# Performance work log

Hardware: AMD Instinct MI355X
Metric: run time of the kernel (lower is better)

## Reference

```python
import jax, jax.numpy as jnp
import numpy as np

B = 4096
T_STEPS = 2048


def setup_inputs() -> dict:
    key = jax.random.key(0)
    k1, k2, k3 = jax.random.split(key, 3)
    inputs = jax.random.normal(k1, (B, T_STEPS), dtype=jnp.float32)
    # replicate torch init: params = rand(t); params /= sum(|params|); alternate signs
    p = jax.random.uniform(k2, (T_STEPS,), dtype=jnp.float32)
    p = p / jnp.sum(jnp.abs(p))
    sign = jnp.where(jnp.arange(T_STEPS) % 2 == 0, jnp.float32(1.0), jnp.float32(-1.0))
    params = p * sign
    bias = jax.random.normal(k3, (1,), dtype=jnp.float32)
    return {"inputs": inputs, "params": params, "bias": bias}


def reference(inputs, params, bias):
    """AR(t) recurrence: for i in [t, 2t): x_i = sum_j x_{i-1-j} * params[j] + bias.
    inputs: [B, t] seed values; returns the t generated values per row, [B, t].
    """
    t_steps = params.shape[0]
    # torch.dot uses inputs reversed (newest first) against params, so the
    # window kept in oldest->newest order pairs with reversed params.
    p_rev = params[::-1]

    def step(window, _):
        # window: [B, t] last t values, oldest -> newest
        new = window @ p_rev + bias[0]  # [B]
        window = jnp.concatenate([window[:, 1:], new[:, None]], axis=1)
        return window, new

    _, outs = jax.lax.scan(step, inputs, None, length=t_steps)
    return outs.T  # [B, t_steps]
```

## Files before the change

kernel.cpp:

```cpp
#include <hip/hip_runtime.h>
#include <hip/hip_bf16.h>

typedef _Float16 f16;
typedef _Float16 f16x8 __attribute__((ext_vector_type(8)));
typedef float f32x4 __attribute__((ext_vector_type(4)));

constexpr int TS = 2048;
constexpr int BB = 4096;

__device__ __forceinline__ int swz4(int c) { return c ^ ((c >> 3) & 7); }

struct ToepShared { char Xs[16384]; char Ws[8192]; };

template <bool REV>
__device__ void toep_body(ToepShared& lds, int w, const f16* __restrict__ Xg,
                          const char* __restrict__ Wg,
                          const float* __restrict__ biasp, void* __restrict__ Yg) {
  char* Xs = lds.Xs;
  char* Ws = lds.Ws;
  const int tid = threadIdx.x;
  const int lane = tid & 63;
  const int wid = tid >> 6;
  const int wrow = (wid >> 1) * 64;
  const int wcol = (wid & 1) * 32;
  const int px = w & 15;
  const int b0 = (w >> 4) * 128;

  float binit = 0.0f;
  if (REV) binit = biasp[0];

  for (int phase = 0; phase < 2; ++phase) {
    const int mblk = phase ? (31 - px) : px;
    const int m0 = mblk * 64;
    const int k0b = REV ? m0 : 0;
    const int k0e = REV ? TS : (m0 + 64);

    f32x4 acc[4][2];
    #pragma unroll
    for (int i = 0; i < 4; ++i)
      #pragma unroll
      for (int j = 0; j < 2; ++j) acc[i][j] = {binit, binit, binit, binit};

    for (int k0 = k0b; k0 < k0e; k0 += 64) {
      __syncthreads();
      #pragma unroll
      for (int t2 = 0; t2 < 4; ++t2) {
        const int t = wid * 4 + t2;
        const int row = t * 8 + (lane >> 3);
        const char* src = (const char*)Xg + ((size_t)(b0 + row) * TS + k0) * 2
                          + (((lane & 7) * 16) ^ ((row & 7) << 4));
        __builtin_amdgcn_global_load_lds(
            (const __attribute__((address_space(1))) unsigned int*)src,
            (__attribute__((address_space(3))) unsigned int*)(Xs + t * 1024),
            16, 0, 0);
      }
      const int dlt = (REV ? (k0 - m0) : (m0 - k0)) >> 6;
      const char* wsrc = Wg + (size_t)dlt * 8192;
      #pragma unroll
      for (int p = 0; p < 2; ++p) {
        const int t = wid * 2 + p;
        __builtin_amdgcn_global_load_lds(
            (const __attribute__((address_space(1))) unsigned int*)(wsrc + t * 1024 + lane * 16),
            (__attribute__((address_space(3))) unsigned int*)(Ws + t * 1024),
            16, 0, 0);
      }
      __syncthreads();

      #pragma unroll
      for (int ks = 0; ks < 2; ++ks) {
        const int colb = ks * 64 + ((lane >> 4) * 16);
        f16x8 af[4], bf[2];
        #pragma unroll
        for (int i = 0; i < 4; ++i) {
          const int row = wrow + i * 16 + (lane & 15);
          af[i] = *(const f16x8*)(Xs + row * 128 + (colb ^ ((row & 7) << 4)));
        }
        #pragma unroll
        for (int j = 0; j < 2; ++j) {
          const int n = wcol + j * 16 + (lane & 15);
          bf[j] = *(const f16x8*)(Ws + n * 128 + (colb ^ ((n & 7) << 4)));
        }
        #pragma unroll
        for (int i = 0; i < 4; ++i)
          #pragma unroll
          for (int j = 0; j < 2; ++j)
            acc[i][j] = __builtin_amdgcn_mfma_f32_16x16x32_f16(
                af[i], bf[j], acc[i][j], 0, 0, 0);
      }
    }

    #pragma unroll
    for (int i = 0; i < 4; ++i) {
      #pragma unroll
      for (int j = 0; j < 2; ++j) {
        #pragma unroll
        for (int r = 0; r < 4; ++r) {
          const int row = b0 + wrow + i * 16 + (lane >> 4) * 4 + r;
          const int col = m0 + wcol + j * 16 + (lane & 15);
          if (REV)
            ((f16*)Yg)[(size_t)row * TS + col] = (f16)acc[i][j][r];
          else
            ((float*)Yg)[(size_t)row * TS + col] = acc[i][j][r];
        }
      }
    }
  }
}

__global__ __launch_bounds__(1024) void prep_kernel(
    const float* __restrict__ X, f16* __restrict__ Xh,
    const float* __restrict__ params, char* __restrict__ Wg) {
  const int b = blockIdx.x;
  const int tid = threadIdx.x;

  if (b < 512) {
    const size_t base = ((size_t)b * 1024 + tid) * 16;
    const float4 a0 = *(const float4*)&X[base];
    const float4 a1 = *(const float4*)&X[base + 4];
    const float4 a2 = *(const float4*)&X[base + 8];
    const float4 a3 = *(const float4*)&X[base + 12];
    f16x8 v0 = {(f16)a0.x, (f16)a0.y, (f16)a0.z, (f16)a0.w,
                (f16)a1.x, (f16)a1.y, (f16)a1.z, (f16)a1.w};
    f16x8 v1 = {(f16)a2.x, (f16)a2.y, (f16)a2.z, (f16)a2.w,
                (f16)a3.x, (f16)a3.y, (f16)a3.z, (f16)a3.w};
    *(f16x8*)&Xh[base] = v0;
    *(f16x8*)&Xh[base + 8] = v1;
    return;
  }

  if (b == 512) {
    const int s2 = tid & 255;
    const int n = s2 >> 2, kq = s2 & 3;
    for (int dlt = tid >> 8; dlt < 32; dlt += 4) {
      char* tile = Wg + (size_t)dlt * 8192;
      #pragma unroll
      for (int part = 0; part < 2; ++part) {
        const int k8 = kq * 16 + part * 8;
        f16x8 v;
        #pragma unroll
        for (int ii = 0; ii < 8; ++ii) {
          const int k = k8 + ii;
          const int dd = dlt * 64 + k - n;
          v[ii] = ((unsigned)dd < (unsigned)TS) ? (f16)params[2047 - dd] : (f16)0.0f;
        }
        *(f16x8*)(tile + n * 128 + ((2 * k8) ^ ((n & 7) << 4))) = v;
      }
    }
    return;
  }

  __shared__ __align__(16) float rp1[2048];
  __shared__ __align__(16) float h_s[2048];
  __shared__ __align__(16) float hist[1024];
  __shared__ __align__(16) float hb[2052];

  const int lane = tid & 63;
  const int wave = tid >> 6;

  if (tid < 512) {
    const int y = tid * 4;
    f32x4 v;
    v[0] = params[2046 - y];
    v[1] = params[2045 - y];
    v[2] = params[2044 - y];
    v[3] = (y + 3 < 2047) ? params[2043 - y] : 0.0f;
    *(f32x4*)&rp1[swz4(tid) * 4] = v;
  }
  __syncthreads();

  if (wave == 0) {
    float hv = (lane == 0) ? 1.0f : 0.0f;
    for (int m = 1; m < 32; ++m) {
      float partial = 0.0f;
      if (lane < m) {
        const int yi = 2047 - m + lane;
        partial = hv * rp1[swz4(yi >> 2) * 4 + (yi & 3)];
      }
      #pragma unroll
      for (int off = 32; off; off >>= 1) partial += __shfl_xor(partial, off);
      if (lane == m) hv = partial;
    }
    if (lane < 32) h_s[lane] = hv;
  }
  __syncthreads();

  const int sub = tid & 7;
  const int gi = tid >> 3;

  for (int n = 32; n < 2048; n <<= 1) {
    const int ng16 = n >> 4;
    const int T = (n >= 128) ? (n >> 7) : 1;

    if (gi < ng16) {
      float acc[16];
      #pragma unroll
      for (int j = 0; j < 16; ++j) acc[j] = 0.0f;
      const int ybase = (2047 - n) - gi * 16 - 15;
      for (int t = 0; t < T; ++t) {
        const int m16 = (sub + 8 * t) * 16;
        if (m16 < n) {
          const int c0 = (ybase + m16) >> 2;
          f32x4 wv[8];
          #pragma unroll
          for (int q = 0; q < 8; ++q) wv[q] = *(const f32x4*)&rp1[swz4(c0 + q) * 4];
          f32x4 hv4[4];
          #pragma unroll
          for (int q = 0; q < 4; ++q) hv4[q] = *(const f32x4*)&h_s[m16 + 4 * q];
          #pragma unroll
          for (int d = 0; d < 16; ++d) {
            const float hd = hv4[d >> 2][d & 3];
            #pragma unroll
            for (int j = 0; j < 16; ++j) {
              const int k = d - j + 15;
              acc[j] += hd * wv[k >> 2][k & 3];
            }
          }
        }
      }
      #pragma unroll
      for (int j = 0; j < 16; ++j) {
        acc[j] += __shfl_xor(acc[j], 1);
        acc[j] += __shfl_xor(acc[j], 2);
        acc[j] += __shfl_xor(acc[j], 4);
      }
      if (sub == 0) {
        #pragma unroll
        for (int q = 0; q < 4; ++q) {
          f32x4 v = {acc[4 * q], acc[4 * q + 1], acc[4 * q + 2], acc[4 * q + 3]};
          *(f32x4*)&hist[gi * 16 + 4 * q] = v;
        }
      }
    }
    __syncthreads();

    const int P = n + 3;
    const int nchunk = (2 * n + 4) >> 2;
    for (int c = tid; c < nchunk; c += 1024) {
      f32x4 v;
      #pragma unroll
      for (int q = 0; q < 4; ++q) {
        const int idx = 4 * c + q - P;
        v[q] = ((unsigned)idx < (unsigned)n) ? hist[idx] : 0.0f;
      }
      *(f32x4*)&hb[swz4(c) * 4] = v;
    }
    __syncthreads();

    if (gi < ng16) {
      float acc[16];
      #pragma unroll
      for (int j = 0; j < 16; ++j) acc[j] = 0.0f;
      int t_end = (gi >= sub) ? (((gi - sub) >> 3) + 1) : 0;
      if (t_end > T) t_end = T;
      const int ybase = P + gi * 16 - 15;
      for (int t = 0; t < t_end; ++t) {
        const int r16 = (sub + 8 * t) * 16;
        const int c0 = (ybase - r16) >> 2;
        f32x4 wv[8];
        #pragma unroll
        for (int q = 0; q < 8; ++q) wv[q] = *(const f32x4*)&hb[swz4(c0 + q) * 4];
        f32x4 hv4[4];
        #pragma unroll
        for (int q = 0; q < 4; ++q) hv4[q] = *(const f32x4*)&h_s[r16 + 4 * q];
        #pragma unroll
        for (int d = 0; d < 16; ++d) {
          const float hd = hv4[d >> 2][d & 3];
          #pragma unroll
          for (int j = 0; j < 16; ++j) {
            const int k = j - d + 15;
            acc[j] += hd * wv[k >> 2][k & 3];
          }
        }
      }
      #pragma unroll
      for (int j = 0; j < 16; ++j) {
        acc[j] += __shfl_xor(acc[j], 1);
        acc[j] += __shfl_xor(acc[j], 2);
        acc[j] += __shfl_xor(acc[j], 4);
      }
      if (sub == 0) {
        #pragma unroll
        for (int q = 0; q < 4; ++q) {
          f32x4 v = {acc[4 * q], acc[4 * q + 1], acc[4 * q + 2], acc[4 * q + 3]};
          *(f32x4*)&h_s[n + gi * 16 + 4 * q] = v;
        }
      }
    }
    __syncthreads();
  }

  {
    const int s2 = tid & 255;
    const int n2 = s2 >> 2, kq = s2 & 3;
    char* WgC = Wg + 32 * 8192;
    for (int dlt = tid >> 8; dlt < 32; dlt += 4) {
      char* tile = WgC + (size_t)dlt * 8192;
      #pragma unroll
      for (int part = 0; part < 2; ++part) {
        const int k8 = kq * 16 + part * 8;
        f16x8 v;
        #pragma unroll
        for (int ii = 0; ii < 8; ++ii) {
          const int k = k8 + ii;
          const int dd = dlt * 64 + n2 - k;
          v[ii] = ((unsigned)dd < (unsigned)TS) ? (f16)h_s[dd] : (f16)0.0f;
        }
        *(f16x8*)(tile + n2 * 128 + ((2 * k8) ^ ((n2 & 7) << 4))) = v;
      }
    }
  }
}

__global__ __launch_bounds__(256, 2) void toep_A(
    const f16* __restrict__ Xh, const char* __restrict__ Wg,
    const float* __restrict__ biasp, f16* __restrict__ u) {
  __shared__ ToepShared lds;
  const int b = blockIdx.x;
  toep_body<true>(lds, (b & 7) * 64 + (b >> 3), Xh, Wg, biasp, (void*)u);
}

__global__ __launch_bounds__(256, 2) void toep_C(
    const f16* __restrict__ u, const char* __restrict__ WgC,
    float* __restrict__ out) {
  __shared__ ToepShared lds;
  const int b = blockIdx.x;
  toep_body<false>(lds, (b & 7) * 64 + (b >> 3), u, WgC, nullptr, (void*)out);
}

extern "C" void kernel_launch(void* const* d_in, const int* in_sizes, int n_in,
                              void* d_out, int out_size, void* d_ws, size_t ws_size,
                              hipStream_t stream) {
  const float* inputs = (const float*)d_in[0];
  const float* params = (const float*)d_in[1];
  const float* bias   = (const float*)d_in[2];
  float* out = (float*)d_out;

  char* ws = (char*)d_ws;
  f16*  Xh = (f16*)ws;
  f16*  u  = (f16*)(ws + (size_t)BB * TS * 2);
  char* Wg = ws + (size_t)BB * TS * 4;

  prep_kernel<<<514, 1024, 0, stream>>>(inputs, Xh, params, Wg);
  toep_A<<<512, 256, 0, stream>>>(Xh, Wg, bias, u);
  toep_C<<<512, 256, 0, stream>>>(u, Wg + 32 * 8192, out);
}
```

Measured before the change: 113.3 us.

## Overlap impulse-response computation with first Toeplitz GEMM in one launch

The serial impulse-response (h) computation moves out of the prep kernel, where a single 1024-thread block was the critical path, into an extra block of the first Toeplitz GEMM kernel. It now runs on 256 threads concurrently with the GEMM tiles. The prep kernel is reshaped into 256-thread blocks, with a separate block per weight tile. Shared memory becomes a union sized to the larger h buffers (about 28KB), which may lower occupancy of the GEMM blocks. The h block with 256 threads may also become a long tail.

After: 118.2 us. +4.2%, slower.

```diff
diff --git a/kernel.cpp b/kernel.cpp
--- a/kernel.cpp
+++ b/kernel.cpp
@@ -11,6 +11,16 @@
 __device__ __forceinline__ int swz4(int c) { return c ^ ((c >> 3) & 7); }
 
 struct ToepShared { char Xs[16384]; char Ws[8192]; };
+
+union MegaShared {
+  ToepShared t;
+  struct {
+    float rp1[2048];
+    float h[2048];
+    float hist[1024];
+    float hbuf[2052];
+  } hb;
+};
 
 template <bool REV>
 __device__ void toep_body(ToepShared& lds, int w, const f16* __restrict__ Xg,
@@ -107,14 +117,174 @@
   }
 }
 
-__global__ __launch_bounds__(1024) void prep_kernel(
+__device__ void h_block_body(MegaShared& lds, const float* __restrict__ params,
+                             char* __restrict__ WgC) {
+  float* rp1 = lds.hb.rp1;
+  float* h_s = lds.hb.h;
+  float* hist = lds.hb.hist;
+  float* hb = lds.hb.hbuf;
+
+  const int tid = threadIdx.x;
+  const int lane = tid & 63;
+  const int wave = tid >> 6;
+
+  for (int c = tid; c < 512; c += 256) {
+    const int y = c * 4;
+    f32x4 v;
+    v[0] = params[2046 - y];
+    v[1] = params[2045 - y];
+    v[2] = params[2044 - y];
+    v[3] = (y + 3 < 2047) ? params[2043 - y] : 0.0f;
+    *(f32x4*)&rp1[swz4(c) * 4] = v;
+  }
+  __syncthreads();
+
+  if (wave == 0) {
+    float hv = (lane == 0) ? 1.0f : 0.0f;
+    for (int m = 1; m < 32; ++m) {
+      float partial = 0.0f;
+      if (lane < m) {
+        const int yi = 2047 - m + lane;
+        partial = hv * rp1[swz4(yi >> 2) * 4 + (yi & 3)];
+      }
+      #pragma unroll
+      for (int off = 32; off; off >>= 1) partial += __shfl_xor(partial, off);
+      if (lane == m) hv = partial;
+    }
+    if (lane < 32) h_s[lane] = hv;
+  }
+  __syncthreads();
+
+  const int sub = tid & 7;
+  const int g0 = tid >> 3;
+
+  for (int n = 32; n < 2048; n <<= 1) {
+    const int ng16 = n >> 4;
+    const int T = (n >= 128) ? (n >> 7) : 1;
+
+    for (int gi = g0; gi < ng16; gi += 32) {
+      float acc[16];
+      #pragma unroll
+      for (int j = 0; j < 16; ++j) acc[j] = 0.0f;
+      const int ybase = (2047 - n) - gi * 16 - 15;
+      for (int t = 0; t < T; ++t) {
+        const int m16 = (sub + 8 * t) * 16;
+        if (m16 < n) {
+          const int c0 = (ybase + m16) >> 2;
+          f32x4 wv[8];
+          #pragma unroll
+          for (int q = 0; q < 8; ++q) wv[q] = *(const f32x4*)&rp1[swz4(c0 + q) * 4];
+          f32x4 hv4[4];
+          #pragma unroll
+          for (int q = 0; q < 4; ++q) hv4[q] = *(const f32x4*)&h_s[m16 + 4 * q];
+          #pragma unroll
+          for (int d = 0; d < 16; ++d) {
+            const float hd = hv4[d >> 2][d & 3];
+            #pragma unroll
+            for (int j = 0; j < 16; ++j) {
+              const int k = d - j + 15;
+              acc[j] += hd * wv[k >> 2][k & 3];
+            }
+          }
+        }
+      }
+      #pragma unroll
+      for (int j = 0; j < 16; ++j) {
+        acc[j] += __shfl_xor(acc[j], 1);
+        acc[j] += __shfl_xor(acc[j], 2);
+        acc[j] += __shfl_xor(acc[j], 4);
+      }
+      if (sub == 0) {
+        #pragma unroll
+        for (int q = 0; q < 4; ++q) {
+          f32x4 v = {acc[4 * q], acc[4 * q + 1], acc[4 * q + 2], acc[4 * q + 3]};
+          *(f32x4*)&hist[gi * 16 + 4 * q] = v;
+        }
+      }
+    }
+    __syncthreads();
+
+    const int P = n + 3;
+    const int nchunk = (2 * n + 4) >> 2;
+    for (int c = tid; c < nchunk; c += 256) {
+      f32x4 v;
+      #pragma unroll
+      for (int q = 0; q < 4; ++q) {
+        const int idx = 4 * c + q - P;
+        v[q] = ((unsigned)idx < (unsigned)n) ? hist[idx] : 0.0f;
+      }
+      *(f32x4*)&hb[swz4(c) * 4] = v;
+    }
+    __syncthreads();
+
+    for (int gi = g0; gi < ng16; gi += 32) {
+      float acc[16];
+      #pragma unroll
+      for (int j = 0; j < 16; ++j) acc[j] = 0.0f;
+      int t_end = (gi >= sub) ? (((gi - sub) >> 3) + 1) : 0;
+      if (t_end > T) t_end = T;
+      const int ybase = P + gi * 16 - 15;
+      for (int t = 0; t < t_end; ++t) {
+        const int r16 = (sub + 8 * t) * 16;
+        const int c0 = (ybase - r16) >> 2;
+        f32x4 wv[8];
+        #pragma unroll
+        for (int q = 0; q < 8; ++q) wv[q] = *(const f32x4*)&hb[swz4(c0 + q) * 4];
+        f32x4 hv4[4];
+        #pragma unroll
+        for (int q = 0; q < 4; ++q) hv4[q] = *(const f32x4*)&h_s[r16 + 4 * q];
+        #pragma unroll
+        for (int d = 0; d < 16; ++d) {
+          const float hd = hv4[d >> 2][d & 3];
+          #pragma unroll
+          for (int j = 0; j < 16; ++j) {
+            const int k = j - d + 15;
+            acc[j] += hd * wv[k >> 2][k & 3];
+          }
+        }
+      }
+      #pragma unroll
+      for (int j = 0; j < 16; ++j) {
+        acc[j] += __shfl_xor(acc[j], 1);
+        acc[j] += __shfl_xor(acc[j], 2);
+        acc[j] += __shfl_xor(acc[j], 4);
+      }
+      if (sub == 0) {
+        #pragma unroll
+        for (int q = 0; q < 4; ++q) {
+          f32x4 v = {acc[4 * q], acc[4 * q + 1], acc[4 * q + 2], acc[4 * q + 3]};
+          *(f32x4*)&h_s[n + gi * 16 + 4 * q] = v;
+        }
+      }
+    }
+    __syncthreads();
+  }
+
+  const int n2 = tid >> 2, kq = tid & 3;
+  for (int dlt = 0; dlt < 32; ++dlt) {
+    char* tile = WgC + (size_t)dlt * 8192;
+    #pragma unroll
+    for (int part = 0; part < 2; ++part) {
+      const int k8 = kq * 16 + part * 8;
+      f16x8 v;
+      #pragma unroll
+      for (int ii = 0; ii < 8; ++ii) {
+        const int k = k8 + ii;
+        const int dd = dlt * 64 + n2 - k;
+        v[ii] = ((unsigned)dd < (unsigned)TS) ? (f16)h_s[dd] : (f16)0.0f;
+      }
+      *(f16x8*)(tile + n2 * 128 + ((2 * k8) ^ ((n2 & 7) << 4))) = v;
+    }
+  }
+}
+
+__global__ __launch_bounds__(256) void conv_prep(
     const float* __restrict__ X, f16* __restrict__ Xh,
     const float* __restrict__ params, char* __restrict__ Wg) {
   const int b = blockIdx.x;
   const int tid = threadIdx.x;
-
-  if (b < 512) {
-    const size_t base = ((size_t)b * 1024 + tid) * 16;
+  if (b < 2048) {
+    const size_t base = ((size_t)b * 256 + tid) * 16;
     const float4 a0 = *(const float4*)&X[base];
     const float4 a1 = *(const float4*)&X[base + 4];
     const float4 a2 = *(const float4*)&X[base + 8];
@@ -125,198 +295,36 @@
                 (f16)a3.x, (f16)a3.y, (f16)a3.z, (f16)a3.w};
     *(f16x8*)&Xh[base] = v0;
     *(f16x8*)&Xh[base + 8] = v1;
+  } else {
+    const int dlt = b - 2048;
+    char* tile = Wg + (size_t)dlt * 8192;
+    const int n = tid >> 2, kq = tid & 3;
+    #pragma unroll
+    for (int part = 0; part < 2; ++part) {
+      const int k8 = kq * 16 + part * 8;
+      f16x8 v;
+      #pragma unroll
+      for (int ii = 0; ii < 8; ++ii) {
+        const int k = k8 + ii;
+        const int dd = dlt * 64 + k - n;
+        v[ii] = ((unsigned)dd < (unsigned)TS) ? (f16)params[2047 - dd] : (f16)0.0f;
+      }
+      *(f16x8*)(tile + n * 128 + ((2 * k8) ^ ((n & 7) << 4))) = v;
+    }
+  }
+}
+
+__global__ __launch_bounds__(256, 2) void mega_A(
+    const f16* __restrict__ Xh, char* __restrict__ Wg,
+    const float* __restrict__ biasp, f16* __restrict__ u,
+    const float* __restrict__ params) {
+  __shared__ MegaShared lds;
+  const int b = blockIdx.x;
+  if (b == 512) {
+    h_block_body(lds, params, Wg + 32 * 8192);
     return;
   }
-
-  if (b == 512) {
-    const int s2 = tid & 255;
-    const int n = s2 >> 2, kq = s2 & 3;
-    for (int dlt = tid >> 8; dlt < 32; dlt += 4) {
-      char* tile = Wg + (size_t)dlt * 8192;
-      #pragma unroll
-      for (int part = 0; part < 2; ++part) {
-        const int k8 = kq * 16 + part * 8;
-        f16x8 v;
-        #pragma unroll
-        for (int ii = 0; ii < 8; ++ii) {
-          const int k = k8 + ii;
-          const int dd = dlt * 64 + k - n;
-          v[ii] = ((unsigned)dd < (unsigned)TS) ? (f16)params[2047 - dd] : (f16)0.0f;
-        }
-        *(f16x8*)(tile + n * 128 + ((2 * k8) ^ ((n & 7) << 4))) = v;
-      }
-    }
-    return;
-  }
-
-  __shared__ __align__(16) float rp1[2048];
-  __shared__ __align__(16) float h_s[2048];
-  __shared__ __align__(16) float hist[1024];
-  __shared__ __align__(16) float hb[2052];
-
-  const int lane = tid & 63;
-  const int wave = tid >> 6;
-
-  if (tid < 512) {
-    const int y = tid * 4;
-    f32x4 v;
-    v[0] = params[2046 - y];
-    v[1] = params[2045 - y];
-    v[2] = params[2044 - y];
-    v[3] = (y + 3 < 2047) ? params[2043 - y] : 0.0f;
-    *(f32x4*)&rp1[swz4(tid) * 4] = v;
-  }
-  __syncthreads();
-
-  if (wave == 0) {
-    float hv = (lane == 0) ? 1.0f : 0.0f;
-    for (int m = 1; m < 32; ++m) {
-      float partial = 0.0f;
-      if (lane < m) {
-        const int yi = 2047 - m + lane;
-        partial = hv * rp1[swz4(yi >> 2) * 4 + (yi & 3)];
-      }
-      #pragma unroll
-      for (int off = 32; off; off >>= 1) partial += __shfl_xor(partial, off);
-      if (lane == m) hv = partial;
-    }
-    if (lane < 32) h_s[lane] = hv;
-  }
-  __syncthreads();
-
-  const int sub = tid & 7;
-  const int gi = tid >> 3;
-
-  for (int n = 32; n < 2048; n <<= 1) {
-    const int ng16 = n >> 4;
-    const int T = (n >= 128) ? (n >> 7) : 1;
-
-    if (gi < ng16) {
-      float acc[16];
-      #pragma unroll
-      for (int j = 0; j < 16; ++j) acc[j] = 0.0f;
-      const int ybase = (2047 - n) - gi * 16 - 15;
-      for (int t = 0; t < T; ++t) {
-        const int m16 = (sub + 8 * t) * 16;
-        if (m16 < n) {
-          const int c0 = (ybase + m16) >> 2;
-          f32x4 wv[8];
-          #pragma unroll
-          for (int q = 0; q < 8; ++q) wv[q] = *(const f32x4*)&rp1[swz4(c0 + q) * 4];
-          f32x4 hv4[4];
-          #pragma unroll
-          for (int q = 0; q < 4; ++q) hv4[q] = *(const f32x4*)&h_s[m16 + 4 * q];
-          #pragma unroll
-          for (int d = 0; d < 16; ++d) {
-            const float hd = hv4[d >> 2][d & 3];
-            #pragma unroll
-            for (int j = 0; j < 16; ++j) {
-              const int k = d - j + 15;
-              acc[j] += hd * wv[k >> 2][k & 3];
-            }
-          }
-        }
-      }
-      #pragma unroll
-      for (int j = 0; j < 16; ++j) {
-        acc[j] += __shfl_xor(acc[j], 1);
-        acc[j] += __shfl_xor(acc[j], 2);
-        acc[j] += __shfl_xor(acc[j], 4);
-      }
-      if (sub == 0) {
-        #pragma unroll
-        for (int q = 0; q < 4; ++q) {
-          f32x4 v = {acc[4 * q], acc[4 * q + 1], acc[4 * q + 2], acc[4 * q + 3]};
-          *(f32x4*)&hist[gi * 16 + 4 * q] = v;
-        }
-      }
-    }
-    __syncthreads();
-
-    const int P = n + 3;
-    const int nchunk = (2 * n + 4) >> 2;
-    for (int c = tid; c < nchunk; c += 1024) {
-      f32x4 v;
-      #pragma unroll
-      for (int q = 0; q < 4; ++q) {
-        const int idx = 4 * c + q - P;
-        v[q] = ((unsigned)idx < (unsigned)n) ? hist[idx] : 0.0f;
-      }
-      *(f32x4*)&hb[swz4(c) * 4] = v;
-    }
-    __syncthreads();
-
-    if (gi < ng16) {
-      float acc[16];
-      #pragma unroll
-      for (int j = 0; j < 16; ++j) acc[j] = 0.0f;
-      int t_end = (gi >= sub) ? (((gi - sub) >> 3) + 1) : 0;
-      if (t_end > T) t_end = T;
-      const int ybase = P + gi * 16 - 15;
-      for (int t = 0; t < t_end; ++t) {
-        const int r16 = (sub + 8 * t) * 16;
-        const int c0 = (ybase - r16) >> 2;
-        f32x4 wv[8];
-        #pragma unroll
-        for (int q = 0; q < 8; ++q) wv[q] = *(const f32x4*)&hb[swz4(c0 + q) * 4];
-        f32x4 hv4[4];
-        #pragma unroll
-        for (int q = 0; q < 4; ++q) hv4[q] = *(const f32x4*)&h_s[r16 + 4 * q];
-        #pragma unroll
-        for (int d = 0; d < 16; ++d) {
-          const float hd = hv4[d >> 2][d & 3];
-          #pragma unroll
-          for (int j = 0; j < 16; ++j) {
-            const int k = j - d + 15;
-            acc[j] += hd * wv[k >> 2][k & 3];
-          }
-        }
-      }
-      #pragma unroll
-      for (int j = 0; j < 16; ++j) {
-        acc[j] += __shfl_xor(acc[j], 1);
-        acc[j] += __shfl_xor(acc[j], 2);
-        acc[j] += __shfl_xor(acc[j], 4);
-      }
-      if (sub == 0) {
-        #pragma unroll
-        for (int q = 0; q < 4; ++q) {
-          f32x4 v = {acc[4 * q], acc[4 * q + 1], acc[4 * q + 2], acc[4 * q + 3]};
-          *(f32x4*)&h_s[n + gi * 16 + 4 * q] = v;
-        }
-      }
-    }
-    __syncthreads();
-  }
-
-  {
-    const int s2 = tid & 255;
-    const int n2 = s2 >> 2, kq = s2 & 3;
-    char* WgC = Wg + 32 * 8192;
-    for (int dlt = tid >> 8; dlt < 32; dlt += 4) {
-      char* tile = WgC + (size_t)dlt * 8192;
-      #pragma unroll
-      for (int part = 0; part < 2; ++part) {
-        const int k8 = kq * 16 + part * 8;
-        f16x8 v;
-        #pragma unroll
-        for (int ii = 0; ii < 8; ++ii) {
-          const int k = k8 + ii;
-          const int dd = dlt * 64 + n2 - k;
-          v[ii] = ((unsigned)dd < (unsigned)TS) ? (f16)h_s[dd] : (f16)0.0f;
-        }
-        *(f16x8*)(tile + n2 * 128 + ((2 * k8) ^ ((n2 & 7) << 4))) = v;
-      }
-    }
-  }
-}
-
-__global__ __launch_bounds__(256, 2) void toep_A(
-    const f16* __restrict__ Xh, const char* __restrict__ Wg,
-    const float* __restrict__ biasp, f16* __restrict__ u) {
-  __shared__ ToepShared lds;
-  const int b = blockIdx.x;
-  toep_body<true>(lds, (b & 7) * 64 + (b >> 3), Xh, Wg, biasp, (void*)u);
+  toep_body<true>(lds.t, (b & 7) * 64 + (b >> 3), Xh, Wg, biasp, (void*)u);
 }
 
 __global__ __launch_bounds__(256, 2) void toep_C(
@@ -340,7 +348,7 @@
   f16*  u  = (f16*)(ws + (size_t)BB * TS * 2);
   char* Wg = ws + (size_t)BB * TS * 4;
 
-  prep_kernel<<<514, 1024, 0, stream>>>(inputs, Xh, params, Wg);
-  toep_A<<<512, 256, 0, stream>>>(Xh, Wg, bias, u);
+  conv_prep<<<2080, 256, 0, stream>>>(inputs, Xh, params, Wg);
+  mega_A<<<513, 256, 0, stream>>>(Xh, Wg, bias, u, params);
   toep_C<<<512, 256, 0, stream>>>(u, Wg + 32 * 8192, out);
 }
```
